# Performance work log

Measured on AMD Instinct MI355X. Metric: run time of the kernel, lower is better.

Reference implementation:

```python
import jax, jax.numpy as jnp
import numpy as np

Q, C, D = 4096, 4096, 1024
EPS = 1e-6  # torch.nn.PairwiseDistance default eps, added to (x1 - x2)


def _cdist_l2(a, b):
    # ||(a + EPS) - b||_2 for all pairs, via GEMM formulation.
    a = a + EPS
    sq = (jnp.sum(a * a, axis=1)[:, None]
          + jnp.sum(b * b, axis=1)[None, :]
          - 2.0 * a @ b.T)
    return jnp.sqrt(jnp.maximum(sq, 0.0))


def setup_inputs() -> dict:
    key = jax.random.key(0)
    k1, k2, k3, k4, k5, k6 = jax.random.split(key, 6)
    return {
        "context_rgb_features": jax.random.normal(k1, (C, D), dtype=jnp.float32),
        "context_flow_features": jax.random.normal(k2, (C, D), dtype=jnp.float32),
        "target_rgb_features": jax.random.normal(k3, (Q, D), dtype=jnp.float32),
        "target_flow_features": jax.random.normal(k4, (Q, D), dtype=jnp.float32),
        "c_r": jax.random.uniform(k5, (Q,), dtype=jnp.float32, minval=0.1, maxval=1.0),
        "c_f": jax.random.uniform(k6, (Q,), dtype=jnp.float32, minval=0.1, maxval=1.0),
    }


def reference(context_rgb_features, context_flow_features,
              target_rgb_features, target_flow_features, c_r, c_f):
    denom = c_r + c_f
    w_r = (c_r / denom)[:, None]   # [Q, 1]
    w_f = (c_f / denom)[:, None]
    d_rgb = _cdist_l2(target_rgb_features, context_rgb_features)    # [Q, C]
    d_flow = _cdist_l2(target_flow_features, context_flow_features)  # [Q, C]
    posterior = w_r * jnp.exp(-d_rgb) + w_f * jnp.exp(-d_flow)
    return posterior / jnp.sum(posterior, axis=1, keepdims=True)
```

## Files before the change

### kernel.cpp

```cpp
#include <hip/hip_runtime.h>
#include <hip/hip_bf16.h>

#define QN 4096
#define CN 4096
#define DN 1024
#define EPSV 1e-6f

#define BM 128
#define BN 128
#define BK 64
#define TILE (BM * BK)

#define MATSZ ((size_t)QN * DN)

using bf16x8 = __attribute__((ext_vector_type(8))) __bf16;
using f32x4  = __attribute__((ext_vector_type(4))) float;

static __device__ __forceinline__ unsigned short f2bf_rne(float x) {
  unsigned int u = __float_as_uint(x);
  unsigned int r = (u + 0x7FFFu + ((u >> 16) & 1u)) >> 16;
  return (unsigned short)r;
}
static __device__ __forceinline__ float bf2f(unsigned short h) {
  return __uint_as_float(((unsigned int)h) << 16);
}

static __device__ __forceinline__ void gload_lds16(const unsigned short* g, unsigned short* l) {
  __builtin_amdgcn_global_load_lds(
      (const __attribute__((address_space(1))) unsigned int*)g,
      (__attribute__((address_space(3))) unsigned int*)l, 16, 0, 0);
}


__global__ void prep_kernel(const float* __restrict__ tgt_r, const float* __restrict__ tgt_f,
                            const float* __restrict__ ctx_r, const float* __restrict__ ctx_f,
                            unsigned short* __restrict__ ws16, float* __restrict__ norms) {
  const int row = blockIdx.x;
  const int mat = blockIdx.y;
  const int t = threadIdx.x;
  const float* src; float eps;
  switch (mat) {
    case 0:  src = tgt_r; eps = EPSV; break;
    case 1:  src = tgt_f; eps = EPSV; break;
    case 2:  src = ctx_r; eps = 0.f;  break;
    default: src = ctx_f; eps = 0.f;  break;
  }
  unsigned short* hi = ws16 + (size_t)mat * MATSZ;
  float* nrm = norms + (size_t)mat * QN;
  const size_t base = (size_t)row * DN;
  float4 v = ((const float4*)(src + base))[t];
  float a[4] = {v.x + eps, v.y + eps, v.z + eps, v.w + eps};
  float ss = 0.f;
  unsigned short hh[4];
#pragma unroll
  for (int k = 0; k < 4; ++k) {
    hh[k] = f2bf_rne(a[k]);
    float f = bf2f(hh[k]);
    ss += f * f;
  }
  ((ushort4*)(hi + base))[t] = make_ushort4(hh[0], hh[1], hh[2], hh[3]);

#pragma unroll
  for (int o = 32; o > 0; o >>= 1) ss += __shfl_down(ss, o);
  __shared__ float red[4];
  if ((t & 63) == 0) red[t >> 6] = ss;
  __syncthreads();
  if (t == 0) nrm[row] = red[0] + red[1] + red[2] + red[3];
}

__global__ __launch_bounds__(256, 2)
void gemm_kernel(const unsigned short* __restrict__ ws16,
                 const float* __restrict__ norms,
                 const float* __restrict__ c_r, const float* __restrict__ c_f,
                 float* __restrict__ out) {
  __shared__ unsigned short S[4 * TILE];

  const int t = threadIdx.x;
  const int lane = t & 63;
  const int wid = t >> 6;
  const int wr = wid >> 1;
  const int wc = wid & 1;
  const int row0 = blockIdx.y * BM;
  const int col0 = blockIdx.x * BN;

  f32x4 acc[2][4][4];
#pragma unroll
  for (int m = 0; m < 2; ++m)
#pragma unroll
    for (int i = 0; i < 4; ++i)
#pragma unroll
      for (int j = 0; j < 4; ++j)
        acc[m][i][j] = (f32x4){0.f, 0.f, 0.f, 0.f};

  const int srw = lane >> 3;
  const int sch = (lane & 7) ^ srw;
  const size_t src_off = (size_t)(wid * 8 + srw) * DN + sch * 8;
  const size_t aoff = (size_t)row0 * DN + src_off;
  const size_t boff = (size_t)col0 * DN + src_off;
  unsigned short* ldsW = S + wid * 8 * BK;

  const unsigned short* pAr = ws16 + 0 * MATSZ + aoff;
  const unsigned short* pAf = ws16 + 1 * MATSZ + aoff;
  const unsigned short* pBr = ws16 + 2 * MATSZ + boff;
  const unsigned short* pBf = ws16 + 3 * MATSZ + boff;

  const int lr = lane & 15;
  const int lq = lane >> 4;
  const int sc0 = (lq ^ (lr & 7)) * 8;
  int ra[4], rb[4];
#pragma unroll
  for (int i = 0; i < 4; ++i) {
    ra[i] = (wr * 64 + i * 16 + lr) * BK + sc0;
    rb[i] = (wc * 64 + i * 16 + lr) * BK + sc0;
  }
#define KS1(x) ((x) ^ 32)

  for (int kc = 0; kc < DN / BK; ++kc) {
    const int k = kc * BK;
    __syncthreads();
#pragma unroll
    for (int it = 0; it < 4; ++it) {
      const size_t g = (size_t)it * 32 * DN + k;
      unsigned short* l = ldsW + it * 32 * BK;
      gload_lds16(pAr + g, l + 0 * TILE);
      gload_lds16(pAf + g, l + 1 * TILE);
      gload_lds16(pBr + g, l + 2 * TILE);
      gload_lds16(pBf + g, l + 3 * TILE);
    }
    __syncthreads();

#pragma unroll
    for (int ksub = 0; ksub < 2; ++ksub) {
      bf16x8 ar[4], af[4], br[4], bf[4];
#pragma unroll
      for (int i = 0; i < 4; ++i) {
        const int oa = ksub ? KS1(ra[i]) : ra[i];
        const int ob = ksub ? KS1(rb[i]) : rb[i];
        ar[i] = *(const bf16x8*)(S + 0 * TILE + oa);
        af[i] = *(const bf16x8*)(S + 1 * TILE + oa);
        br[i] = *(const bf16x8*)(S + 2 * TILE + ob);
        bf[i] = *(const bf16x8*)(S + 3 * TILE + ob);
      }
#pragma unroll
      for (int i = 0; i < 4; ++i)
#pragma unroll
        for (int j = 0; j < 4; ++j) {
          acc[0][i][j] = __builtin_amdgcn_mfma_f32_16x16x32_bf16(ar[i], br[j], acc[0][i][j], 0, 0, 0);
          acc[1][i][j] = __builtin_amdgcn_mfma_f32_16x16x32_bf16(af[i], bf[j], acc[1][i][j], 0, 0, 0);
        }
    }
  }

  const float* tn_r = norms;
  const float* tn_f = norms + QN;
  const float* cn_r = norms + 2 * QN;
  const float* cn_f = norms + 3 * QN;

#pragma unroll
  for (int i = 0; i < 4; ++i) {
#pragma unroll
    for (int r = 0; r < 4; ++r) {
      const int tq = row0 + wr * 64 + i * 16 + lq * 4 + r;
      const float tnr = tn_r[tq];
      const float tnf = tn_f[tq];
      const float cr = c_r[tq], cf = c_f[tq];
      const float inv = 1.f / (cr + cf);
      const float wgr = cr * inv, wgf = cf * inv;
#pragma unroll
      for (int j = 0; j < 4; ++j) {
        const int cc = col0 + wc * 64 + j * 16 + lr;
        const float sr_ = tnr + cn_r[cc] - 2.f * acc[0][i][j][r];
        const float sf_ = tnf + cn_f[cc] - 2.f * acc[1][i][j][r];
        const float dr = sqrtf(fmaxf(sr_, 0.f));
        const float df = sqrtf(fmaxf(sf_, 0.f));
        const float p = wgr * __expf(-dr) + wgf * __expf(-df);
        out[(size_t)tq * CN + cc] = p;
      }
    }
  }
}

__global__ void norm_kernel(float* __restrict__ out) {
  const int row = blockIdx.x;
  const int t = threadIdx.x;
  float4* p = (float4*)(out + (size_t)row * CN);
  float4 v[4];
  float s = 0.f;
#pragma unroll
  for (int i = 0; i < 4; ++i) {
    v[i] = p[t + 256 * i];
    s += v[i].x + v[i].y + v[i].z + v[i].w;
  }
#pragma unroll
  for (int o = 32; o > 0; o >>= 1) s += __shfl_down(s, o);
  __shared__ float red[4];
  if ((t & 63) == 0) red[t >> 6] = s;
  __syncthreads();
  const float inv = 1.f / (red[0] + red[1] + red[2] + red[3]);
#pragma unroll
  for (int i = 0; i < 4; ++i) {
    v[i].x *= inv; v[i].y *= inv; v[i].z *= inv; v[i].w *= inv;
    p[t + 256 * i] = v[i];
  }
}

extern "C" void kernel_launch(void* const* d_in, const int* in_sizes, int n_in,
                              void* d_out, int out_size, void* d_ws, size_t ws_size,
                              hipStream_t stream) {
  const float* ctx_r = (const float*)d_in[0];
  const float* ctx_f = (const float*)d_in[1];
  const float* tgt_r = (const float*)d_in[2];
  const float* tgt_f = (const float*)d_in[3];
  const float* c_r   = (const float*)d_in[4];
  const float* c_f   = (const float*)d_in[5];
  float* out = (float*)d_out;
  unsigned short* ws16 = (unsigned short*)d_ws;
  float* norms = (float*)(ws16 + 4 * MATSZ);

  prep_kernel<<<dim3(QN, 4), 256, 0, stream>>>(tgt_r, tgt_f, ctx_r, ctx_f, ws16, norms);
  gemm_kernel<<<dim3(CN / BN, QN / BM), 256, 0, stream>>>(ws16, norms, c_r, c_f, out);
  norm_kernel<<<QN, 256, 0, stream>>>(out);
}
```

Baseline: 218.4 us.

## Warp-specialize GEMM with producer waves double-buffering LDS tiles

The GEMM block grows from 256 to 512 threads. Four producer waves stream bf16 tiles into a double-buffered LDS array with direct global-to-LDS loads, while four consumer waves run the MFMA loop on the other buffer. BK is halved to 32 and the LDS swizzle and fragment addressing are rebuilt for the new layout. The aim is to overlap global loads with compute, but 512-thread blocks at two blocks per CU cut the register budget per wave, which risks accumulator spills. The scheme also depends on barriers waiting for the async LDS loads to finish.

```diff
diff --git a/kernel.cpp b/kernel.cpp
--- a/kernel.cpp
+++ b/kernel.cpp
@@ -8,7 +8,7 @@
 
 #define BM 128
 #define BN 128
-#define BK 64
+#define BK 32
 #define TILE (BM * BK)
 
 #define MATSZ ((size_t)QN * DN)
@@ -68,20 +68,48 @@
   if (t == 0) nrm[row] = red[0] + red[1] + red[2] + red[3];
 }
 
-__global__ __launch_bounds__(256, 2)
+__global__ __launch_bounds__(512, 2)
 void gemm_kernel(const unsigned short* __restrict__ ws16,
                  const float* __restrict__ norms,
                  const float* __restrict__ c_r, const float* __restrict__ c_f,
                  float* __restrict__ out) {
-  __shared__ unsigned short S[4 * TILE];
+  __shared__ unsigned short S[2][4 * TILE];
 
   const int t = threadIdx.x;
   const int lane = t & 63;
   const int wid = t >> 6;
+  const int row0 = blockIdx.y * BM;
+  const int col0 = blockIdx.x * BN;
+
+  if (wid >= 4) {
+    const int tl = wid - 4;
+    const unsigned short* base = ws16 + (size_t)tl * MATSZ
+                               + (size_t)(tl < 2 ? row0 : col0) * DN;
+    const int po = (lane & 7) ^ (lane >> 3);
+    const int r0 = 2 * (lane >> 3) + (po >> 2);
+    const int c0 = (po & 3) * 8;
+    const unsigned short* src = base + (size_t)r0 * DN + c0;
+    unsigned short* dst0 = &S[0][tl * TILE];
+
+#pragma unroll
+    for (int i = 0; i < 8; ++i)
+      gload_lds16(src + (size_t)i * 16 * DN, dst0 + i * 512);
+
+    for (int kc = 0; kc < DN / BK; ++kc) {
+      __syncthreads();
+      if (kc + 1 < DN / BK) {
+        const unsigned short* s2 = src + (kc + 1) * BK;
+        unsigned short* d2 = &S[(kc + 1) & 1][tl * TILE];
+#pragma unroll
+        for (int i = 0; i < 8; ++i)
+          gload_lds16(s2 + (size_t)i * 16 * DN, d2 + i * 512);
+      }
+    }
+    return;
+  }
+
   const int wr = wid >> 1;
   const int wc = wid & 1;
-  const int row0 = blockIdx.y * BM;
-  const int col0 = blockIdx.x * BN;
 
   f32x4 acc[2][4][4];
 #pragma unroll
@@ -92,63 +120,34 @@
       for (int j = 0; j < 4; ++j)
         acc[m][i][j] = (f32x4){0.f, 0.f, 0.f, 0.f};
 
-  const int srw = lane >> 3;
-  const int sch = (lane & 7) ^ srw;
-  const size_t src_off = (size_t)(wid * 8 + srw) * DN + sch * 8;
-  const size_t aoff = (size_t)row0 * DN + src_off;
-  const size_t boff = (size_t)col0 * DN + src_off;
-  unsigned short* ldsW = S + wid * 8 * BK;
-
-  const unsigned short* pAr = ws16 + 0 * MATSZ + aoff;
-  const unsigned short* pAf = ws16 + 1 * MATSZ + aoff;
-  const unsigned short* pBr = ws16 + 2 * MATSZ + boff;
-  const unsigned short* pBf = ws16 + 3 * MATSZ + boff;
-
   const int lr = lane & 15;
   const int lq = lane >> 4;
-  const int sc0 = (lq ^ (lr & 7)) * 8;
+  const int pos = (lq + 4 * (lr & 1)) ^ (lr >> 1);
   int ra[4], rb[4];
 #pragma unroll
   for (int i = 0; i < 4; ++i) {
-    ra[i] = (wr * 64 + i * 16 + lr) * BK + sc0;
-    rb[i] = (wc * 64 + i * 16 + lr) * BK + sc0;
-  }
-#define KS1(x) ((x) ^ 32)
+    ra[i] = (wr * 32 + i * 8 + (lr >> 1)) * 64 + pos * 8;
+    rb[i] = (wc * 32 + i * 8 + (lr >> 1)) * 64 + pos * 8;
+  }
 
   for (int kc = 0; kc < DN / BK; ++kc) {
-    const int k = kc * BK;
     __syncthreads();
-#pragma unroll
-    for (int it = 0; it < 4; ++it) {
-      const size_t g = (size_t)it * 32 * DN + k;
-      unsigned short* l = ldsW + it * 32 * BK;
-      gload_lds16(pAr + g, l + 0 * TILE);
-      gload_lds16(pAf + g, l + 1 * TILE);
-      gload_lds16(pBr + g, l + 2 * TILE);
-      gload_lds16(pBf + g, l + 3 * TILE);
+    const unsigned short* Sb = &S[kc & 1][0];
+    bf16x8 ar[4], af[4], br[4], bf[4];
+#pragma unroll
+    for (int i = 0; i < 4; ++i) {
+      ar[i] = *(const bf16x8*)(Sb + 0 * TILE + ra[i]);
+      af[i] = *(const bf16x8*)(Sb + 1 * TILE + ra[i]);
+      br[i] = *(const bf16x8*)(Sb + 2 * TILE + rb[i]);
+      bf[i] = *(const bf16x8*)(Sb + 3 * TILE + rb[i]);
     }
-    __syncthreads();
-
-#pragma unroll
-    for (int ksub = 0; ksub < 2; ++ksub) {
-      bf16x8 ar[4], af[4], br[4], bf[4];
-#pragma unroll
-      for (int i = 0; i < 4; ++i) {
-        const int oa = ksub ? KS1(ra[i]) : ra[i];
-        const int ob = ksub ? KS1(rb[i]) : rb[i];
-        ar[i] = *(const bf16x8*)(S + 0 * TILE + oa);
-        af[i] = *(const bf16x8*)(S + 1 * TILE + oa);
-        br[i] = *(const bf16x8*)(S + 2 * TILE + ob);
-        bf[i] = *(const bf16x8*)(S + 3 * TILE + ob);
+#pragma unroll
+    for (int i = 0; i < 4; ++i)
+#pragma unroll
+      for (int j = 0; j < 4; ++j) {
+        acc[0][i][j] = __builtin_amdgcn_mfma_f32_16x16x32_bf16(ar[i], br[j], acc[0][i][j], 0, 0, 0);
+        acc[1][i][j] = __builtin_amdgcn_mfma_f32_16x16x32_bf16(af[i], bf[j], acc[1][i][j], 0, 0, 0);
       }
-#pragma unroll
-      for (int i = 0; i < 4; ++i)
-#pragma unroll
-        for (int j = 0; j < 4; ++j) {
-          acc[0][i][j] = __builtin_amdgcn_mfma_f32_16x16x32_bf16(ar[i], br[j], acc[0][i][j], 0, 0, 0);
-          acc[1][i][j] = __builtin_amdgcn_mfma_f32_16x16x32_bf16(af[i], bf[j], acc[1][i][j], 0, 0, 0);
-        }
-    }
   }
 
   const float* tn_r = norms;
@@ -218,6 +217,6 @@
   float* norms = (float*)(ws16 + 4 * MATSZ);
 
   prep_kernel<<<dim3(QN, 4), 256, 0, stream>>>(tgt_r, tgt_f, ctx_r, ctx_f, ws16, norms);
-  gemm_kernel<<<dim3(CN / BN, QN / BM), 256, 0, stream>>>(ws16, norms, c_r, c_f, out);
+  gemm_kernel<<<dim3(CN / BN, QN / BM), 512, 0, stream>>>(ws16, norms, c_r, c_f, out);
   norm_kernel<<<QN, 256, 0, stream>>>(out);
 }
```

Result: slower. 257.5 us (+17.9%).

## Add producer warps with double-buffered LDS and swizzled block mapping

Applied to the files above, without the earlier changes.

The GEMM kernel now uses warp specialization. Four extra producer waves stream bf16 tiles into a double-buffered LDS ring through global_load_lds, while four consumer waves run MFMA. The rgb and flow GEMMs run as two sequential phases over the same buffers instead of loading all four tiles per k-step. The grid becomes 1D with a swizzled block-to-tile mapping for better L2 reuse. The goal is to overlap global loads with MFMA work and halve the LDS footprint per stage, at the cost of a 512-thread block and a barrier in every iteration.

```diff
diff --git a/kernel.cpp b/kernel.cpp
--- a/kernel.cpp
+++ b/kernel.cpp
@@ -68,20 +68,52 @@
   if (t == 0) nrm[row] = red[0] + red[1] + red[2] + red[3];
 }
 
-__global__ __launch_bounds__(256, 2)
+__global__ __launch_bounds__(512, 2)
 void gemm_kernel(const unsigned short* __restrict__ ws16,
                  const float* __restrict__ norms,
                  const float* __restrict__ c_r, const float* __restrict__ c_f,
                  float* __restrict__ out) {
-  __shared__ unsigned short S[4 * TILE];
+  __shared__ unsigned short S[2][2][TILE];
 
   const int t = threadIdx.x;
   const int lane = t & 63;
   const int wid = t >> 6;
+
+  const int b = blockIdx.x;
+  const int row0 = (b >> 5) * BM;
+  const int col0 = (((b & 7) << 2) | ((b >> 3) & 3)) * BN;
+
+  if (wid >= 4) {
+    const int pw = wid - 4;
+    const int tl = pw >> 1;
+    const int half = pw & 1;
+    const int srw = lane >> 3;
+    const int sch = (lane & 7) ^ srw;
+    const size_t rbase = (size_t)((tl ? col0 : row0) + half * 64) * DN;
+    const unsigned short* m0 = ws16 + (size_t)(tl * 2) * MATSZ + rbase
+                             + (size_t)srw * DN + sch * 8;
+    unsigned short* d0 = &S[0][tl][half * 64 * BK];
+
+#define STAGE(it)                                                            \
+    {                                                                        \
+      const int ph = (it) >> 4;                                              \
+      const unsigned short* sP = m0 + (size_t)ph * MATSZ + ((it) & 15) * BK; \
+      unsigned short* dP = d0 + ((it) & 1) * (2 * TILE);                     \
+      _Pragma("unroll")                                                      \
+      for (int i = 0; i < 8; ++i)                                            \
+        gload_lds16(sP + (size_t)i * 8 * DN, dP + i * 512);                  \
+    }
+
+    STAGE(0);
+    for (int it = 0; it < 32; ++it) {
+      __syncthreads();
+      if (it < 31) STAGE(it + 1);
+    }
+    return;
+  }
+
   const int wr = wid >> 1;
   const int wc = wid & 1;
-  const int row0 = blockIdx.y * BM;
-  const int col0 = blockIdx.x * BN;
 
   f32x4 acc[2][4][4];
 #pragma unroll
@@ -91,18 +123,6 @@
 #pragma unroll
       for (int j = 0; j < 4; ++j)
         acc[m][i][j] = (f32x4){0.f, 0.f, 0.f, 0.f};
-
-  const int srw = lane >> 3;
-  const int sch = (lane & 7) ^ srw;
-  const size_t src_off = (size_t)(wid * 8 + srw) * DN + sch * 8;
-  const size_t aoff = (size_t)row0 * DN + src_off;
-  const size_t boff = (size_t)col0 * DN + src_off;
-  unsigned short* ldsW = S + wid * 8 * BK;
-
-  const unsigned short* pAr = ws16 + 0 * MATSZ + aoff;
-  const unsigned short* pAf = ws16 + 1 * MATSZ + aoff;
-  const unsigned short* pBr = ws16 + 2 * MATSZ + boff;
-  const unsigned short* pBf = ws16 + 3 * MATSZ + boff;
 
   const int lr = lane & 15;
   const int lq = lane >> 4;
@@ -115,38 +135,26 @@
   }
 #define KS1(x) ((x) ^ 32)
 
-  for (int kc = 0; kc < DN / BK; ++kc) {
-    const int k = kc * BK;
-    __syncthreads();
-#pragma unroll
-    for (int it = 0; it < 4; ++it) {
-      const size_t g = (size_t)it * 32 * DN + k;
-      unsigned short* l = ldsW + it * 32 * BK;
-      gload_lds16(pAr + g, l + 0 * TILE);
-      gload_lds16(pAf + g, l + 1 * TILE);
-      gload_lds16(pBr + g, l + 2 * TILE);
-      gload_lds16(pBf + g, l + 3 * TILE);
-    }
-    __syncthreads();
-
-#pragma unroll
-    for (int ksub = 0; ksub < 2; ++ksub) {
-      bf16x8 ar[4], af[4], br[4], bf[4];
+#pragma unroll
+  for (int phase = 0; phase < 2; ++phase) {
+    for (int kc = 0; kc < 16; ++kc) {
+      __syncthreads();
+      const unsigned short* Sa = &S[(phase * 16 + kc) & 1][0][0];
+      const unsigned short* Sb = &S[(phase * 16 + kc) & 1][1][0];
+      bf16x8 a0[4], a1[4], b0[4], b1[4];
 #pragma unroll
       for (int i = 0; i < 4; ++i) {
-        const int oa = ksub ? KS1(ra[i]) : ra[i];
-        const int ob = ksub ? KS1(rb[i]) : rb[i];
-        ar[i] = *(const bf16x8*)(S + 0 * TILE + oa);
-        af[i] = *(const bf16x8*)(S + 1 * TILE + oa);
-        br[i] = *(const bf16x8*)(S + 2 * TILE + ob);
-        bf[i] = *(const bf16x8*)(S + 3 * TILE + ob);
+        a0[i] = *(const bf16x8*)(Sa + ra[i]);
+        a1[i] = *(const bf16x8*)(Sa + KS1(ra[i]));
+        b0[i] = *(const bf16x8*)(Sb + rb[i]);
+        b1[i] = *(const bf16x8*)(Sb + KS1(rb[i]));
       }
 #pragma unroll
       for (int i = 0; i < 4; ++i)
 #pragma unroll
         for (int j = 0; j < 4; ++j) {
-          acc[0][i][j] = __builtin_amdgcn_mfma_f32_16x16x32_bf16(ar[i], br[j], acc[0][i][j], 0, 0, 0);
-          acc[1][i][j] = __builtin_amdgcn_mfma_f32_16x16x32_bf16(af[i], bf[j], acc[1][i][j], 0, 0, 0);
+          acc[phase][i][j] = __builtin_amdgcn_mfma_f32_16x16x32_bf16(a0[i], b0[j], acc[phase][i][j], 0, 0, 0);
+          acc[phase][i][j] = __builtin_amdgcn_mfma_f32_16x16x32_bf16(a1[i], b1[j], acc[phase][i][j], 0, 0, 0);
         }
     }
   }
@@ -218,6 +226,6 @@
   float* norms = (float*)(ws16 + 4 * MATSZ);
 
   prep_kernel<<<dim3(QN, 4), 256, 0, stream>>>(tgt_r, tgt_f, ctx_r, ctx_f, ws16, norms);
-  gemm_kernel<<<dim3(CN / BN, QN / BM), 256, 0, stream>>>(ws16, norms, c_r, c_f, out);
+  gemm_kernel<<<dim3(1024), 512, 0, stream>>>(ws16, norms, c_r, c_f, out);
   norm_kernel<<<QN, 256, 0, stream>>>(out);
 }
```

Result: slower. 242.7 us (+11.2%).
